# Kernel tuning notes

Measured on AMD Instinct MI355X. Metric: run time of the kernel, lower is better.

## Reference

```python
import jax, jax.numpy as jnp
import numpy as np

C = 192   # channels (class attr)
N = 196   # tokens per stream; 2N = 392, R feat dim = 784
B = 256

def _pw(x, w, b):
    # 1x1 Conv1d == pointwise channel mix: x [B,Ci,L] -> [B,Co,L]
    return jnp.einsum('oi,bil->bol', w, x) + b[None, :, None]

def _bn(x, g, beta, m, v):
    # eval-mode BatchNorm1d
    inv = g / jnp.sqrt(v + 1e-5)
    return (x - m[None, :, None]) * inv[None, :, None] + beta[None, :, None]

def setup_inputs():
    key = jax.random.key(0)
    ks = jax.random.split(key, 24)
    s = 1.0 / np.sqrt(C)
    d = {}
    d['x'] = jax.random.normal(ks[0], (B, N, C), dtype=jnp.float32)
    d['y'] = jax.random.normal(ks[1], (B, N, C), dtype=jnp.float32)
    # linear_conv_1: Conv1d(C,C,1) + BN + ReLU
    d['w1'] = jax.random.normal(ks[2], (C, C), dtype=jnp.float32) * s
    d['b1'] = jax.random.normal(ks[3], (C,), dtype=jnp.float32) * 0.01
    d['g1'] = jnp.ones((C,), jnp.float32)
    d['be1'] = jnp.zeros((C,), jnp.float32)
    d['m1'] = jax.random.normal(ks[4], (C,), dtype=jnp.float32) * 0.1
    d['v1'] = jax.random.uniform(ks[5], (C,), dtype=jnp.float32) + 0.5
    # linear_conv_2
    d['w2'] = jax.random.normal(ks[6], (C, C), dtype=jnp.float32) * s
    d['b2'] = jax.random.normal(ks[7], (C,), dtype=jnp.float32) * 0.01
    d['g2'] = jnp.ones((C,), jnp.float32)
    d['be2'] = jnp.zeros((C,), jnp.float32)
    d['m2'] = jax.random.normal(ks[8], (C,), dtype=jnp.float32) * 0.1
    d['v2'] = jax.random.uniform(ks[9], (C,), dtype=jnp.float32) + 0.5
    # linear_conv_3: Conv1d(C,C,1)
    d['w3'] = jax.random.normal(ks[10], (C, C), dtype=jnp.float32) * s
    d['b3'] = jax.random.normal(ks[11], (C,), dtype=jnp.float32) * 0.01
    # linear_conv_4: Conv1d(784,784,1)
    d['w4'] = jax.random.normal(ks[12], (784, 784), dtype=jnp.float32) / np.sqrt(784)
    d['b4'] = jax.random.normal(ks[13], (784,), dtype=jnp.float32) * 0.01
    # linear_conv_5: Conv1d(C+784,1,1)
    d['w5'] = jax.random.normal(ks[14], (1, C + 784), dtype=jnp.float32) / np.sqrt(C + 784)
    d['b5'] = jax.random.normal(ks[15], (1,), dtype=jnp.float32) * 0.01
    return d

def reference(x, y, w1, b1, g1, be1, m1, v1, w2, b2, g2, be2, m2, v2, w3, b3, w4, b4, w5, b5):
    xp = jnp.swapaxes(x, 1, 2)  # [B,C,N]
    yp = jnp.swapaxes(y, 1, 2)
    phi_x = jax.nn.relu(_bn(_pw(xp, w1, b1), g1, be1, m1, v1))
    phi_y = jax.nn.relu(_bn(_pw(yp, w2, b2), g2, be2, m2, v2))
    cat_phi = jnp.concatenate([phi_x, phi_y], axis=2)            # [B,C,2N]
    A = jnp.einsum('bcn,bcm->bnm', cat_phi, cat_phi)             # [B,2N,2N]
    # R[b,i,:] = cat(A[b,i,:], A[b,:,i]) for i in 0..2N-1, then permute(0,2,1)
    R = jnp.concatenate([A, jnp.swapaxes(A, 1, 2)], axis=2)      # [B,2N,4N]
    R = jnp.swapaxes(R, 1, 2)                                    # [B,4N,2N] = [B,784,392]
    v = _pw(cat_phi, w3, b3)                                     # [B,C,392]
    v_ = _pw(R, w4, b4)                                          # [B,784,392]
    cat_v = jnp.concatenate([v, v_], axis=1)                     # [B,976,392]
    W = _pw(cat_v, w5, b5)                                       # [B,1,392]
    out = xp * W[:, :, :N] + yp * W[:, :, N:]                    # [B,C,N]
    return out
```

## Files before the change

### kernel.cpp

```cpp
#include <hip/hip_runtime.h>
#include <hip/hip_bf16.h>

typedef __attribute__((ext_vector_type(8))) short bf16x8;
typedef __attribute__((ext_vector_type(4))) float f32x4;

#define CDIM 192
#define NTOK 196
#define LTOT 392
#define NBE 64

__device__ __forceinline__ ushort f2bf(float f) {
  uint u = __float_as_uint(f);
  u = (u + 0x7FFFu + ((u >> 16) & 1u)) >> 16;
  return (ushort)u;
}
__device__ __forceinline__ float bf2f(ushort h) {
  return __uint_as_float(((uint)h) << 16);
}
__device__ __forceinline__ uint pk2(float lo, float hi) {
  __hip_bfloat162 t = __float22bfloat162_rn(float2{lo, hi});
  uint r;
  __builtin_memcpy(&r, &t, 4);
  return r;
}
__device__ __forceinline__ float wave_reduce(float a) {
#pragma unroll
  for (int off = 32; off > 0; off >>= 1) a += __shfl_xor(a, off);
  return a;
}
__device__ __forceinline__ void barL() {
  asm volatile("s_waitcnt lgkmcnt(0)" ::: "memory");
  __builtin_amdgcn_s_barrier();
  __builtin_amdgcn_sched_barrier(0);
}

__global__ __launch_bounds__(256) void prep_kernel(
    const float* __restrict__ w1, const float* __restrict__ b1, const float* __restrict__ g1,
    const float* __restrict__ be1, const float* __restrict__ m1, const float* __restrict__ v1,
    const float* __restrict__ w2, const float* __restrict__ b2, const float* __restrict__ g2,
    const float* __restrict__ be2, const float* __restrict__ m2, const float* __restrict__ v2,
    const float* __restrict__ w3, const float* __restrict__ b3,
    const float* __restrict__ w4, const float* __restrict__ b4,
    const float* __restrict__ w5, const float* __restrict__ b5,
    ushort* __restrict__ w1b, ushort* __restrict__ w2b,
    float* __restrict__ u3, float* __restrict__ u4, float* __restrict__ cvecs,
    float* __restrict__ Kc) {
  const int bid = blockIdx.x;
  const int wid = threadIdx.x >> 6, lane = threadIdx.x & 63;
  if (bid < NBE) {
    for (int i = bid * 256 + threadIdx.x; i < 74112; i += NBE * 256) {
      if (i < 36864) {
        int o = i / CDIM;
        float inv = g1[o] * rsqrtf(v1[o] + 1e-5f);
        w1b[i] = f2bf(w1[i] * inv);
      } else if (i < 73728) {
        int j = i - 36864; int o = j / CDIM;
        float inv = g2[o] * rsqrtf(v2[o] + 1e-5f);
        w2b[j] = f2bf(w2[j] * inv);
      } else {
        int k = i - 73728; int h = k / CDIM, o = k % CDIM;
        const float* bb = h ? b2 : b1; const float* gg = h ? g2 : g1;
        const float* bee = h ? be2 : be1;
        const float* mm = h ? m2 : m1; const float* vv = h ? v2 : v1;
        float inv = gg[o] * rsqrtf(vv[o] + 1e-5f);
        cvecs[k] = (bb[o] - mm[o]) * inv + bee[o];
      }
    }
  } else if (bid < NBE + 48) {
    int j = (bid - NBE) * 4 + wid;
    float a = 0.f;
    for (int c = lane; c < CDIM; c += 64) a += w5[c] * w3[c * CDIM + j];
    a = wave_reduce(a);
    if (lane == 0) u3[j] = a;
  } else if (bid < NBE + 48 + 98) {
    int j = (bid - NBE - 48) * 4 + wid;
    float a = 0.f;
    for (int o = lane; o < 784; o += 64)
      a += w5[CDIM + o] * (w4[o * 784 + j] + w4[o * 784 + j + LTOT]);
    a = wave_reduce(a);
    if (lane == 0) u4[j] = a;
  } else {
    if (wid == 0) {
      float a = 0.f;
      for (int i = lane; i < CDIM + 784; i += 64)
        a += (i < CDIM) ? w5[i] * b3[i] : w5[i] * b4[i - CDIM];
      a = wave_reduce(a);
      if (lane == 0) Kc[0] = a + b5[0];
    }
  }
}

#define PHIL_BYTES (404 * 384)
#define OFF_U4S PHIL_BYTES
#define OFF_CSL (OFF_U4S + 1600)
#define OFF_SARR (OFF_CSL + 1536)
#define SMEM_BYTES (OFF_SARR + 768)

extern __shared__ char smem[];

__global__ __launch_bounds__(768, 1) void fused_kernel(
    const float* __restrict__ x, const float* __restrict__ y,
    const ushort* __restrict__ w1b, const ushort* __restrict__ w2b,
    const float* __restrict__ cvecs, const float* __restrict__ u4,
    const float* __restrict__ u3, const float* __restrict__ Kc,
    float* __restrict__ Wg) {
  const int b = blockIdx.x;
  ushort* phiL = (ushort*)smem;
  float* u4s = (float*)(smem + OFF_U4S);
  float* csL = (float*)(smem + OFF_CSL);
  float* sArr = (float*)(smem + OFF_SARR);
  const int tid = threadIdx.x;
  for (int i = tid; i < 400; i += 768) u4s[i] = (i < LTOT) ? u4[i] : 0.f;
  for (int i = tid; i < 384; i += 768) csL[i] = cvecs[i];

  const int w = tid >> 6, lane = tid & 63;
  const int lrow = lane & 15, kgrp = lane >> 4;
  const int c = w * 16 + lrow;

  bf16x8 bfr0[6], bfr1[6];
#pragma unroll
  for (int kk = 0; kk < 6; kk++) {
    bfr0[kk] = *(const bf16x8*)(w1b + (size_t)c * CDIM + kk * 32 + kgrp * 8);
    bfr1[kk] = *(const bf16x8*)(w2b + (size_t)c * CDIM + kk * 32 + kgrp * 8);
  }
  barL();
  const float csr0 = csL[c], csr1 = csL[CDIM + c];

  const float4* xb4 = (const float4*)(x + (size_t)b * NTOK * CDIM);
  const float4* yb4 = (const float4*)(y + (size_t)b * NTOK * CDIM);
  float sp = 0.f;

  auto loadpf = [&](int R, float4* pf) {
    if (R < 14) {
      const float4* s4 = (R < 7) ? xb4 : yb4;
      const int base = (R % 7) * 1536;
#pragma unroll
      for (int p = 0; p < 2; p++) {
        const int fi = base + p * 768 + tid;
        pf[p] = (fi < 9408) ? s4[fi] : float4{0.f, 0.f, 0.f, 0.f};
      }
    }
  };
  float4 pfA[2], pfB[2];
  loadpf(0, pfA);
  loadpf(1, pfB);

  for (int R = 0; R < 14; R++) {
    const int h = R / 7, r = R % 7;
#pragma unroll
    for (int p = 0; p < 2; p++) {
      const int fi = r * 1536 + p * 768 + tid;
      if (fi < 9408) {
        const int row = fi / 48, c4 = fi - row * 48;
        const int l = h * NTOK + row;
        uint2 wv;
        wv.x = pk2(pfA[p].x, pfA[p].y);
        wv.y = pk2(pfA[p].z, pfA[p].w);
        uint addr = (uint)(l * 384 + c4 * 8) ^ (uint)((l & 7) << 4);
        *(uint2*)((char*)phiL + addr) = wv;
      }
    }
    pfA[0] = pfB[0]; pfA[1] = pfB[1];
    loadpf(R + 2, pfB);
    barL();

    const bool t1ok = (r * 32 + 16) < NTOK;
    f32x4 acc0 = {0.f, 0.f, 0.f, 0.f}, acc1 = {0.f, 0.f, 0.f, 0.f};
    {
      bf16x8 a0[6], a1[6];
      const int l0 = h * NTOK + r * 32 + lrow;
#pragma unroll
      for (int kk = 0; kk < 6; kk++) {
        uint ad0 = (uint)(l0 * 384 + (kk * 32 + kgrp * 8) * 2) ^ (uint)((l0 & 7) << 4);
        a0[kk] = *(const bf16x8*)((const char*)phiL + ad0);
        const int l1 = l0 + 16;
        uint ad1 = (uint)(l1 * 384 + (kk * 32 + kgrp * 8) * 2) ^ (uint)((l1 & 7) << 4);
        a1[kk] = *(const bf16x8*)((const char*)phiL + ad1);
      }
      if (h == 0) {
#pragma unroll
        for (int kk = 0; kk < 6; kk++) {
          acc0 = __builtin_amdgcn_mfma_f32_16x16x32_bf16(a0[kk], bfr0[kk], acc0, 0, 0, 0);
          if (t1ok) acc1 = __builtin_amdgcn_mfma_f32_16x16x32_bf16(a1[kk], bfr0[kk], acc1, 0, 0, 0);
        }
      } else {
#pragma unroll
        for (int kk = 0; kk < 6; kk++) {
          acc0 = __builtin_amdgcn_mfma_f32_16x16x32_bf16(a0[kk], bfr1[kk], acc0, 0, 0, 0);
          if (t1ok) acc1 = __builtin_amdgcn_mfma_f32_16x16x32_bf16(a1[kk], bfr1[kk], acc1, 0, 0, 0);
        }
      }
    }
    barL();

    {
      const float csr = h ? csr1 : csr0;
#pragma unroll
      for (int tt = 0; tt < 2; tt++) {
        const int rb = r * 32 + tt * 16;
        if (rb < NTOK) {
          const f32x4 ac = tt ? acc1 : acc0;
          const float v0 = fmaxf(ac[0] + csr, 0.f);
          const float v1 = fmaxf(ac[1] + csr, 0.f);
          const float v2 = fmaxf(ac[2] + csr, 0.f);
          const float v3 = fmaxf(ac[3] + csr, 0.f);
          const uint p01 = pk2(v0, v1), p23 = pk2(v2, v3);
          const int row0 = rb + 4 * kgrp;
#pragma unroll
          for (int j = 0; j < 4; j++) {
            const int row = row0 + j;
            if (row < NTOK) {
              const int l = h * NTOK + row;
              uint addr = (uint)(l * 384 + c * 2) ^ (uint)((l & 7) << 4);
              const uint piece = (j == 0) ? (p01 & 0xFFFFu) : (j == 1) ? (p01 >> 16)
                               : (j == 2) ? (p23 & 0xFFFFu) : (p23 >> 16);
              *(ushort*)((char*)phiL + addr) = (ushort)piece;
              const float vj = (j == 0) ? v0 : (j == 1) ? v1 : (j == 2) ? v2 : v3;
              sp += u4s[l] * vj;
            }
          }
        }
      }
    }
  }

  sp += __shfl_xor(sp, 16);
  sp += __shfl_xor(sp, 32);
  if (kgrp == 0) sArr[c] = sp;
  barL();
  for (int i = tid; i < CDIM; i += 768) sArr[i] = u3[i] + sArr[i];
  barL();

  const float Kv = Kc[0];
  const int grp = tid >> 2, g4 = tid & 3;
  for (int l = grp; l < LTOT; l += 192) {
    float acc = 0.f;
#pragma unroll
    for (int q = 0; q < 12; q++) {
      const int cc = g4 * 48 + q * 4;
      uint addr = (uint)(l * 384 + cc * 2) ^ (uint)((l & 7) << 4);
      ushort4 v = *(const ushort4*)((const char*)phiL + addr);
      acc += sArr[cc] * bf2f(v.x) + sArr[cc + 1] * bf2f(v.y) +
             sArr[cc + 2] * bf2f(v.z) + sArr[cc + 3] * bf2f(v.w);
    }
    acc += __shfl_xor(acc, 1);
    acc += __shfl_xor(acc, 2);
    if (g4 == 0) Wg[b * LTOT + l] = acc + Kv;
  }
}

__global__ __launch_bounds__(256) void out_kernel(
    const float* __restrict__ x, const float* __restrict__ y,
    const float* __restrict__ Wg, float* __restrict__ out) {
  const int bid = blockIdx.x;
  const int b = bid / 7, nt = bid % 7;
  const int n0 = nt * 28;
  __shared__ float Wl[56];
  __shared__ float tile[28][193];
  const int tid = threadIdx.x;
  if (tid < 56) {
    const int lg = (tid < 28) ? (n0 + tid) : (NTOK + n0 + tid - 28);
    Wl[tid] = Wg[b * LTOT + lg];
  }
  __syncthreads();
  for (int i = tid; i < 28 * 48; i += 256) {
    const int nl = i / 48, c4 = (i % 48) * 4;
    const size_t xi = ((size_t)b * NTOK + n0 + nl) * CDIM + c4;
    const float4 xv = *(const float4*)&x[xi];
    const float4 yv = *(const float4*)&y[xi];
    const float wx = Wl[nl], wy = Wl[28 + nl];
    tile[nl][c4 + 0] = xv.x * wx + yv.x * wy;
    tile[nl][c4 + 1] = xv.y * wx + yv.y * wy;
    tile[nl][c4 + 2] = xv.z * wx + yv.z * wy;
    tile[nl][c4 + 3] = xv.w * wx + yv.w * wy;
  }
  __syncthreads();
  for (int i = tid; i < CDIM * 7; i += 256) {
    const int c = i / 7, nq = i % 7;
    float4 o;
    o.x = tile[nq * 4 + 0][c]; o.y = tile[nq * 4 + 1][c];
    o.z = tile[nq * 4 + 2][c]; o.w = tile[nq * 4 + 3][c];
    *(float4*)&out[((size_t)b * CDIM + c) * NTOK + n0 + nq * 4] = o;
  }
}

extern "C" void kernel_launch(void* const* d_in, const int* in_sizes, int n_in,
                              void* d_out, int out_size, void* d_ws, size_t ws_size,
                              hipStream_t stream) {
  const float* x   = (const float*)d_in[0];
  const float* y   = (const float*)d_in[1];
  const float* w1  = (const float*)d_in[2];
  const float* b1  = (const float*)d_in[3];
  const float* g1  = (const float*)d_in[4];
  const float* be1 = (const float*)d_in[5];
  const float* m1  = (const float*)d_in[6];
  const float* v1  = (const float*)d_in[7];
  const float* w2  = (const float*)d_in[8];
  const float* b2  = (const float*)d_in[9];
  const float* g2  = (const float*)d_in[10];
  const float* be2 = (const float*)d_in[11];
  const float* m2  = (const float*)d_in[12];
  const float* v2  = (const float*)d_in[13];
  const float* w3  = (const float*)d_in[14];
  const float* b3  = (const float*)d_in[15];
  const float* w4  = (const float*)d_in[16];
  const float* b4  = (const float*)d_in[17];
  const float* w5  = (const float*)d_in[18];
  const float* b5  = (const float*)d_in[19];
  float* out = (float*)d_out;

  char* ws = (char*)d_ws;
  ushort* w1b  = (ushort*)ws;
  ushort* w2b  = (ushort*)(ws + 73728);
  float* fbase = (float*)(ws + 147456);
  float* u3    = fbase;
  float* u4    = fbase + 192;
  float* cvecs = fbase + 584;
  float* Kc    = fbase + 968;
  float* Wg    = fbase + 976;

  prep_kernel<<<211, 256, 0, stream>>>(w1, b1, g1, be1, m1, v1,
                                       w2, b2, g2, be2, m2, v2,
                                       w3, b3, w4, b4, w5, b5,
                                       w1b, w2b, u3, u4, cvecs, Kc);
  fused_kernel<<<256, 768, SMEM_BYTES, stream>>>(x, y, w1b, w2b, cvecs, u4,
                                                 u3, Kc, Wg);
  out_kernel<<<256 * 7, 256, 0, stream>>>(x, y, Wg, out);
}
```

Baseline: 63.42 us.

## Fuse output scaling into main kernel and widen per-round row tiles

Removes the separate out_kernel launch: the fused kernel keeps the per-token gate W in shared memory and itself computes out = x*Wx + y*Wy, then transposes through a padded LDS tile with prefetched x/y loads. The phi projection loop also shifts from 14 rounds of 32 rows to 8 rounds of 64 rows, each round handling four 16-row MFMA tiles. This saves a kernel launch, the global round-trip of Wg and fewer barriers. In exchange the output phase now runs on only 256 blocks instead of 1792, which may lower memory-level parallelism, and register pressure rises.

```diff
diff --git a/kernel.cpp b/kernel.cpp
--- a/kernel.cpp
+++ b/kernel.cpp
@@ -92,9 +92,10 @@
 
 #define PHIL_BYTES (404 * 384)
 #define OFF_U4S PHIL_BYTES
-#define OFF_CSL (OFF_U4S + 1600)
+#define OFF_CSL (OFF_U4S + 1632)
 #define OFF_SARR (OFF_CSL + 1536)
-#define SMEM_BYTES (OFF_SARR + 768)
+#define OFF_WL (OFF_SARR + 768)
+#define SMEM_BYTES (OFF_WL + 1568)
 
 extern __shared__ char smem[];
 
@@ -103,14 +104,15 @@
     const ushort* __restrict__ w1b, const ushort* __restrict__ w2b,
     const float* __restrict__ cvecs, const float* __restrict__ u4,
     const float* __restrict__ u3, const float* __restrict__ Kc,
-    float* __restrict__ Wg) {
+    float* __restrict__ out) {
   const int b = blockIdx.x;
   ushort* phiL = (ushort*)smem;
   float* u4s = (float*)(smem + OFF_U4S);
   float* csL = (float*)(smem + OFF_CSL);
   float* sArr = (float*)(smem + OFF_SARR);
+  float* Wl = (float*)(smem + OFF_WL);
   const int tid = threadIdx.x;
-  for (int i = tid; i < 400; i += 768) u4s[i] = (i < LTOT) ? u4[i] : 0.f;
+  for (int i = tid; i < 408; i += 768) u4s[i] = (i < LTOT) ? u4[i] : 0.f;
   for (int i = tid; i < 384; i += 768) csL[i] = cvecs[i];
 
   const int w = tid >> 6, lane = tid & 63;
@@ -131,25 +133,25 @@
   float sp = 0.f;
 
   auto loadpf = [&](int R, float4* pf) {
-    if (R < 14) {
-      const float4* s4 = (R < 7) ? xb4 : yb4;
-      const int base = (R % 7) * 1536;
-#pragma unroll
-      for (int p = 0; p < 2; p++) {
+    if (R < 8) {
+      const float4* s4 = (R < 4) ? xb4 : yb4;
+      const int base = (R & 3) * 3072;
+#pragma unroll
+      for (int p = 0; p < 4; p++) {
         const int fi = base + p * 768 + tid;
         pf[p] = (fi < 9408) ? s4[fi] : float4{0.f, 0.f, 0.f, 0.f};
       }
     }
   };
-  float4 pfA[2], pfB[2];
+  float4 pfA[4], pfB[4];
   loadpf(0, pfA);
   loadpf(1, pfB);
 
-  for (int R = 0; R < 14; R++) {
-    const int h = R / 7, r = R % 7;
-#pragma unroll
-    for (int p = 0; p < 2; p++) {
-      const int fi = r * 1536 + p * 768 + tid;
+  for (int R = 0; R < 8; R++) {
+    const int h = R >> 2, r = R & 3;
+#pragma unroll
+    for (int p = 0; p < 4; p++) {
+      const int fi = r * 3072 + p * 768 + tid;
       if (fi < 9408) {
         const int row = fi / 48, c4 = fi - row * 48;
         const int l = h * NTOK + row;
@@ -160,64 +162,60 @@
         *(uint2*)((char*)phiL + addr) = wv;
       }
     }
-    pfA[0] = pfB[0]; pfA[1] = pfB[1];
+#pragma unroll
+    for (int p = 0; p < 4; p++) pfA[p] = pfB[p];
     loadpf(R + 2, pfB);
     barL();
 
-    const bool t1ok = (r * 32 + 16) < NTOK;
-    f32x4 acc0 = {0.f, 0.f, 0.f, 0.f}, acc1 = {0.f, 0.f, 0.f, 0.f};
-    {
-      bf16x8 a0[6], a1[6];
-      const int l0 = h * NTOK + r * 32 + lrow;
-#pragma unroll
-      for (int kk = 0; kk < 6; kk++) {
-        uint ad0 = (uint)(l0 * 384 + (kk * 32 + kgrp * 8) * 2) ^ (uint)((l0 & 7) << 4);
-        a0[kk] = *(const bf16x8*)((const char*)phiL + ad0);
-        const int l1 = l0 + 16;
-        uint ad1 = (uint)(l1 * 384 + (kk * 32 + kgrp * 8) * 2) ^ (uint)((l1 & 7) << 4);
-        a1[kk] = *(const bf16x8*)((const char*)phiL + ad1);
-      }
-      if (h == 0) {
+    f32x4 acc[4];
+#pragma unroll
+    for (int tt = 0; tt < 4; tt++) acc[tt] = f32x4{0.f, 0.f, 0.f, 0.f};
+#pragma unroll
+    for (int tt = 0; tt < 4; tt++) {
+      const int rb = r * 64 + tt * 16;
+      if (rb < NTOK) {
+        bf16x8 af[6];
+        const int l0 = h * NTOK + rb + lrow;
 #pragma unroll
         for (int kk = 0; kk < 6; kk++) {
-          acc0 = __builtin_amdgcn_mfma_f32_16x16x32_bf16(a0[kk], bfr0[kk], acc0, 0, 0, 0);
-          if (t1ok) acc1 = __builtin_amdgcn_mfma_f32_16x16x32_bf16(a1[kk], bfr0[kk], acc1, 0, 0, 0);
+          uint ad = (uint)(l0 * 384 + (kk * 32 + kgrp * 8) * 2) ^ (uint)((l0 & 7) << 4);
+          af[kk] = *(const bf16x8*)((const char*)phiL + ad);
         }
-      } else {
-#pragma unroll
-        for (int kk = 0; kk < 6; kk++) {
-          acc0 = __builtin_amdgcn_mfma_f32_16x16x32_bf16(a0[kk], bfr1[kk], acc0, 0, 0, 0);
-          if (t1ok) acc1 = __builtin_amdgcn_mfma_f32_16x16x32_bf16(a1[kk], bfr1[kk], acc1, 0, 0, 0);
+        if (h == 0) {
+#pragma unroll
+          for (int kk = 0; kk < 6; kk++)
+            acc[tt] = __builtin_amdgcn_mfma_f32_16x16x32_bf16(af[kk], bfr0[kk], acc[tt], 0, 0, 0);
+        } else {
+#pragma unroll
+          for (int kk = 0; kk < 6; kk++)
+            acc[tt] = __builtin_amdgcn_mfma_f32_16x16x32_bf16(af[kk], bfr1[kk], acc[tt], 0, 0, 0);
         }
       }
     }
     barL();
 
-    {
-      const float csr = h ? csr1 : csr0;
-#pragma unroll
-      for (int tt = 0; tt < 2; tt++) {
-        const int rb = r * 32 + tt * 16;
-        if (rb < NTOK) {
-          const f32x4 ac = tt ? acc1 : acc0;
-          const float v0 = fmaxf(ac[0] + csr, 0.f);
-          const float v1 = fmaxf(ac[1] + csr, 0.f);
-          const float v2 = fmaxf(ac[2] + csr, 0.f);
-          const float v3 = fmaxf(ac[3] + csr, 0.f);
-          const uint p01 = pk2(v0, v1), p23 = pk2(v2, v3);
-          const int row0 = rb + 4 * kgrp;
-#pragma unroll
-          for (int j = 0; j < 4; j++) {
-            const int row = row0 + j;
-            if (row < NTOK) {
-              const int l = h * NTOK + row;
-              uint addr = (uint)(l * 384 + c * 2) ^ (uint)((l & 7) << 4);
-              const uint piece = (j == 0) ? (p01 & 0xFFFFu) : (j == 1) ? (p01 >> 16)
-                               : (j == 2) ? (p23 & 0xFFFFu) : (p23 >> 16);
-              *(ushort*)((char*)phiL + addr) = (ushort)piece;
-              const float vj = (j == 0) ? v0 : (j == 1) ? v1 : (j == 2) ? v2 : v3;
-              sp += u4s[l] * vj;
-            }
+    const float csr = h ? csr1 : csr0;
+#pragma unroll
+    for (int tt = 0; tt < 4; tt++) {
+      const int rb = r * 64 + tt * 16;
+      if (rb < NTOK) {
+        const float v0 = fmaxf(acc[tt][0] + csr, 0.f);
+        const float v1 = fmaxf(acc[tt][1] + csr, 0.f);
+        const float v2 = fmaxf(acc[tt][2] + csr, 0.f);
+        const float v3 = fmaxf(acc[tt][3] + csr, 0.f);
+        const uint p01 = pk2(v0, v1), p23 = pk2(v2, v3);
+        const int row0 = rb + 4 * kgrp;
+#pragma unroll
+        for (int j = 0; j < 4; j++) {
+          const int row = row0 + j;
+          if (row < NTOK) {
+            const int l = h * NTOK + row;
+            uint addr = (uint)(l * 384 + c * 2) ^ (uint)((l & 7) << 4);
+            const uint piece = (j == 0) ? (p01 & 0xFFFFu) : (j == 1) ? (p01 >> 16)
+                             : (j == 2) ? (p23 & 0xFFFFu) : (p23 >> 16);
+            *(ushort*)((char*)phiL + addr) = (ushort)piece;
+            const float vj = (j == 0) ? v0 : (j == 1) ? v1 : (j == 2) ? v2 : v3;
+            sp += u4s[l] * vj;
           }
         }
       }
@@ -245,42 +243,57 @@
     }
     acc += __shfl_xor(acc, 1);
     acc += __shfl_xor(acc, 2);
-    if (g4 == 0) Wg[b * LTOT + l] = acc + Kv;
-  }
-}
-
-__global__ __launch_bounds__(256) void out_kernel(
-    const float* __restrict__ x, const float* __restrict__ y,
-    const float* __restrict__ Wg, float* __restrict__ out) {
-  const int bid = blockIdx.x;
-  const int b = bid / 7, nt = bid % 7;
-  const int n0 = nt * 28;
-  __shared__ float Wl[56];
-  __shared__ float tile[28][193];
-  const int tid = threadIdx.x;
-  if (tid < 56) {
-    const int lg = (tid < 28) ? (n0 + tid) : (NTOK + n0 + tid - 28);
-    Wl[tid] = Wg[b * LTOT + lg];
-  }
-  __syncthreads();
-  for (int i = tid; i < 28 * 48; i += 256) {
-    const int nl = i / 48, c4 = (i % 48) * 4;
-    const size_t xi = ((size_t)b * NTOK + n0 + nl) * CDIM + c4;
-    const float4 xv = *(const float4*)&x[xi];
-    const float4 yv = *(const float4*)&y[xi];
-    const float wx = Wl[nl], wy = Wl[28 + nl];
-    tile[nl][c4 + 0] = xv.x * wx + yv.x * wy;
-    tile[nl][c4 + 1] = xv.y * wx + yv.y * wy;
-    tile[nl][c4 + 2] = xv.z * wx + yv.z * wy;
-    tile[nl][c4 + 3] = xv.w * wx + yv.w * wy;
-  }
-  __syncthreads();
-  for (int i = tid; i < CDIM * 7; i += 256) {
-    const int c = i / 7, nq = i % 7;
-    float4 o;
-    o.x = tile[nq * 4 + 0][c]; o.y = tile[nq * 4 + 1][c];
-    o.z = tile[nq * 4 + 2][c]; o.w = tile[nq * 4 + 3][c];
-    *(float4*)&out[((size_t)b * CDIM + c) * NTOK + n0 + nq * 4] = o;
+    if (g4 == 0) Wl[l] = acc + Kv;
+  }
+
+  float* tileF = (float*)smem;
+  const float* xb = x + (size_t)b * NTOK * CDIM;
+  const float* yb = y + (size_t)b * NTOK * CDIM;
+  float4 px[2], py[2];
+  auto loadT = [&](int nt) {
+    if (nt < 7) {
+#pragma unroll
+      for (int p = 0; p < 2; p++) {
+        const int i = p * 768 + tid;
+        if (i < 1344) {
+          const size_t xi = (size_t)(nt * 28 + i / 48) * CDIM + (i % 48) * 4;
+          px[p] = *(const float4*)&xb[xi];
+          py[p] = *(const float4*)&yb[xi];
+        }
+      }
+    }
+  };
+  loadT(0);
+  for (int nt = 0; nt < 7; nt++) {
+    const int n0 = nt * 28;
+    barL();
+#pragma unroll
+    for (int p = 0; p < 2; p++) {
+      const int i = p * 768 + tid;
+      if (i < 1344) {
+        const int nl = i / 48, c4 = (i % 48) * 4;
+        const float wx = Wl[n0 + nl], wy = Wl[NTOK + n0 + nl];
+        tileF[nl * 193 + c4 + 0] = px[p].x * wx + py[p].x * wy;
+        tileF[nl * 193 + c4 + 1] = px[p].y * wx + py[p].y * wy;
+        tileF[nl * 193 + c4 + 2] = px[p].z * wx + py[p].z * wy;
+        tileF[nl * 193 + c4 + 3] = px[p].w * wx + py[p].w * wy;
+      }
+    }
+    loadT(nt + 1);
+    barL();
+#pragma unroll
+    for (int p = 0; p < 2; p++) {
+      const int i = p * 768 + tid;
+      if (i < 1344) {
+        const int cc = i / 7, nq = i % 7;
+        float4 o;
+        o.x = tileF[(nq * 4 + 0) * 193 + cc];
+        o.y = tileF[(nq * 4 + 1) * 193 + cc];
+        o.z = tileF[(nq * 4 + 2) * 193 + cc];
+        o.w = tileF[(nq * 4 + 3) * 193 + cc];
+        *(float4*)&out[((size_t)b * CDIM + cc) * NTOK + n0 + nq * 4] = o;
+      }
+    }
   }
 }
 
@@ -317,13 +330,11 @@
   float* u4    = fbase + 192;
   float* cvecs = fbase + 584;
   float* Kc    = fbase + 968;
-  float* Wg    = fbase + 976;
 
   prep_kernel<<<211, 256, 0, stream>>>(w1, b1, g1, be1, m1, v1,
                                        w2, b2, g2, be2, m2, v2,
                                        w3, b3, w4, b4, w5, b5,
                                        w1b, w2b, u3, u4, cvecs, Kc);
   fused_kernel<<<256, 768, SMEM_BYTES, stream>>>(x, y, w1b, w2b, cvecs, u4,
-                                                 u3, Kc, Wg);
-  out_kernel<<<256 * 7, 256, 0, stream>>>(x, y, Wg, out);
-}
+                                                 u3, Kc, out);
+}
```

New measurement: 61.37 us. -3.2%, faster.

## Split fused per-batch kernel into two 1024-block phi passes with recompute

Applied to the files above, without the earlier changes.

Replaces the single 256-block fused kernel, which kept all of phi in shared memory, with two kernels, each launched as 1024 blocks split by batch, stream and token half. The first computes the u4-weighted partial sums of phi. The second recomputes phi with 32x32x16 MFMAs and reduces it against the combined channel coefficients to produce Wg. The aim is to fill the GPU with more, smaller blocks and drop the large shared-memory footprint. The cost is reading x and y twice, doing the phi GEMM twice, and one extra launch.

```diff
diff --git a/kernel.cpp b/kernel.cpp
--- a/kernel.cpp
+++ b/kernel.cpp
@@ -2,7 +2,7 @@
 #include <hip/hip_bf16.h>
 
 typedef __attribute__((ext_vector_type(8))) short bf16x8;
-typedef __attribute__((ext_vector_type(4))) float f32x4;
+typedef __attribute__((ext_vector_type(16))) float f32x16;
 
 #define CDIM 192
 #define NTOK 196
@@ -90,162 +90,173 @@
   }
 }
 
-#define PHIL_BYTES (404 * 384)
-#define OFF_U4S PHIL_BYTES
-#define OFF_CSL (OFF_U4S + 1600)
-#define OFF_SARR (OFF_CSL + 1536)
-#define SMEM_BYTES (OFF_SARR + 768)
-
-extern __shared__ char smem[];
-
-__global__ __launch_bounds__(768, 1) void fused_kernel(
+__device__ __constant__ int L0S[2][4] = {{0, 32, 64, -1}, {96, 128, 160, 164}};
+
+__global__ __launch_bounds__(384) void phis_kernel(
     const float* __restrict__ x, const float* __restrict__ y,
     const ushort* __restrict__ w1b, const ushort* __restrict__ w2b,
     const float* __restrict__ cvecs, const float* __restrict__ u4,
-    const float* __restrict__ u3, const float* __restrict__ Kc,
+    float* __restrict__ s_part) {
+  const int bid = blockIdx.x;
+  const int b = bid >> 2, h = (bid >> 1) & 1, g = bid & 1;
+  const float4* src4 = (const float4*)(((h ? y : x) + (size_t)b * NTOK * CDIM));
+  const ushort* wb = h ? w2b : w1b;
+  __shared__ ushort Abuf[2][32 * CDIM];
+  __shared__ float u4s[100];
+  const int tid = threadIdx.x;
+  const int rbase = g ? 96 : 0;
+  for (int i = tid; i < 100; i += 384) u4s[i] = u4[h * NTOK + rbase + i];
+
+  const int w = tid >> 6, lane = tid & 63;
+  const int cl32 = lane & 31, hi = lane >> 5;
+  const int c = w * 32 + cl32;
+
+  bf16x8 bfr[12];
+#pragma unroll
+  for (int kk = 0; kk < 12; kk++)
+    bfr[kk] = *(const bf16x8*)(wb + (size_t)c * CDIM + kk * 16 + hi * 8);
+  const float csr = cvecs[h * CDIM + c];
+
+  const int nchunks = g ? 4 : 3;
+  float sp = 0.f;
+  float4 pf[4];
+#pragma unroll
+  for (int p = 0; p < 4; p++) pf[p] = src4[L0S[g][0] * 48 + p * 384 + tid];
+
+  for (int k = 0; k < 4; k++) {
+    if (k >= nchunks) break;
+    const int l0 = L0S[g][k];
+    ushort* Ab = &Abuf[k & 1][0];
+#pragma unroll
+    for (int p = 0; p < 4; p++) {
+      const int fi = p * 384 + tid;
+      const int r = fi / 48, c4 = fi % 48;
+      uint2 wv;
+      wv.x = pk2(pf[p].x, pf[p].y);
+      wv.y = pk2(pf[p].z, pf[p].w);
+      uint addr = (uint)(r * 384 + c4 * 8) ^ (uint)((r & 7) << 4);
+      *(uint2*)((char*)Ab + addr) = wv;
+    }
+    if (k + 1 < nchunks) {
+#pragma unroll
+      for (int p = 0; p < 4; p++)
+        pf[p] = src4[L0S[g][k + 1] * 48 + p * 384 + tid];
+    }
+    __builtin_amdgcn_sched_barrier(0);
+    barL();
+    f32x16 acc;
+#pragma unroll
+    for (int e = 0; e < 16; e++) acc[e] = 0.f;
+    const uint swz = (uint)((cl32 & 7) << 4);
+    __builtin_amdgcn_s_setprio(1);
+#pragma unroll
+    for (int kk = 0; kk < 12; kk++) {
+      uint ad = (uint)(cl32 * 384 + kk * 32 + hi * 16) ^ swz;
+      bf16x8 af = *(const bf16x8*)((const char*)Ab + ad);
+      acc = __builtin_amdgcn_mfma_f32_32x32x16_bf16(af, bfr[kk], acc, 0, 0, 0);
+    }
+    __builtin_amdgcn_s_setprio(0);
+    const bool ovl = (l0 == 164);
+#pragma unroll
+    for (int e = 0; e < 16; e++) {
+      const int rl = (e & 3) + 8 * (e >> 2) + 4 * hi;
+      const int row = l0 + rl;
+      if (!ovl || row >= 192) {
+        const float v = fmaxf(acc[e] + csr, 0.f);
+        sp += u4s[row - rbase] * v;
+      }
+    }
+  }
+  sp += __shfl_xor(sp, 32);
+  if (hi == 0) s_part[(size_t)((b * 2 + h) * 2 + g) * CDIM + c] = sp;
+}
+
+__global__ __launch_bounds__(384) void wrec_kernel(
+    const float* __restrict__ x, const float* __restrict__ y,
+    const ushort* __restrict__ w1b, const ushort* __restrict__ w2b,
+    const float* __restrict__ cvecs, const float* __restrict__ u3,
+    const float* __restrict__ s_part, const float* __restrict__ Kc,
     float* __restrict__ Wg) {
-  const int b = blockIdx.x;
-  ushort* phiL = (ushort*)smem;
-  float* u4s = (float*)(smem + OFF_U4S);
-  float* csL = (float*)(smem + OFF_CSL);
-  float* sArr = (float*)(smem + OFF_SARR);
+  const int bid = blockIdx.x;
+  const int b = bid >> 2, h = (bid >> 1) & 1, g = bid & 1;
+  const float4* src4 = (const float4*)(((h ? y : x) + (size_t)b * NTOK * CDIM));
+  const ushort* wb = h ? w2b : w1b;
+  __shared__ ushort Abuf[2][32 * CDIM];
+  __shared__ float Wred[6][32];
   const int tid = threadIdx.x;
-  for (int i = tid; i < 400; i += 768) u4s[i] = (i < LTOT) ? u4[i] : 0.f;
-  for (int i = tid; i < 384; i += 768) csL[i] = cvecs[i];
-
   const int w = tid >> 6, lane = tid & 63;
-  const int lrow = lane & 15, kgrp = lane >> 4;
-  const int c = w * 16 + lrow;
-
-  bf16x8 bfr0[6], bfr1[6];
-#pragma unroll
-  for (int kk = 0; kk < 6; kk++) {
-    bfr0[kk] = *(const bf16x8*)(w1b + (size_t)c * CDIM + kk * 32 + kgrp * 8);
-    bfr1[kk] = *(const bf16x8*)(w2b + (size_t)c * CDIM + kk * 32 + kgrp * 8);
-  }
-  barL();
-  const float csr0 = csL[c], csr1 = csL[CDIM + c];
-
-  const float4* xb4 = (const float4*)(x + (size_t)b * NTOK * CDIM);
-  const float4* yb4 = (const float4*)(y + (size_t)b * NTOK * CDIM);
-  float sp = 0.f;
-
-  auto loadpf = [&](int R, float4* pf) {
-    if (R < 14) {
-      const float4* s4 = (R < 7) ? xb4 : yb4;
-      const int base = (R % 7) * 1536;
-#pragma unroll
-      for (int p = 0; p < 2; p++) {
-        const int fi = base + p * 768 + tid;
-        pf[p] = (fi < 9408) ? s4[fi] : float4{0.f, 0.f, 0.f, 0.f};
+  const int cl32 = lane & 31, hi = lane >> 5;
+  const int c = w * 32 + cl32;
+
+  bf16x8 bfr[12];
+#pragma unroll
+  for (int kk = 0; kk < 12; kk++)
+    bfr[kk] = *(const bf16x8*)(wb + (size_t)c * CDIM + kk * 16 + hi * 8);
+  const float csr = cvecs[h * CDIM + c];
+  float cf = u3[c];
+#pragma unroll
+  for (int q = 0; q < 4; q++) cf += s_part[(size_t)(b * 4 + q) * CDIM + c];
+  const float Kv = Kc[0];
+
+  const int nchunks = g ? 4 : 3;
+  float4 pf[4];
+#pragma unroll
+  for (int p = 0; p < 4; p++) pf[p] = src4[L0S[g][0] * 48 + p * 384 + tid];
+
+  for (int k = 0; k < 4; k++) {
+    if (k >= nchunks) break;
+    const int l0 = L0S[g][k];
+    ushort* Ab = &Abuf[k & 1][0];
+#pragma unroll
+    for (int p = 0; p < 4; p++) {
+      const int fi = p * 384 + tid;
+      const int r = fi / 48, c4 = fi % 48;
+      uint2 wv;
+      wv.x = pk2(pf[p].x, pf[p].y);
+      wv.y = pk2(pf[p].z, pf[p].w);
+      uint addr = (uint)(r * 384 + c4 * 8) ^ (uint)((r & 7) << 4);
+      *(uint2*)((char*)Ab + addr) = wv;
+    }
+    if (k + 1 < nchunks) {
+#pragma unroll
+      for (int p = 0; p < 4; p++)
+        pf[p] = src4[L0S[g][k + 1] * 48 + p * 384 + tid];
+    }
+    __builtin_amdgcn_sched_barrier(0);
+    barL();
+    f32x16 acc;
+#pragma unroll
+    for (int e = 0; e < 16; e++) acc[e] = 0.f;
+    const uint swz = (uint)((cl32 & 7) << 4);
+    __builtin_amdgcn_s_setprio(1);
+#pragma unroll
+    for (int kk = 0; kk < 12; kk++) {
+      uint ad = (uint)(cl32 * 384 + kk * 32 + hi * 16) ^ swz;
+      bf16x8 af = *(const bf16x8*)((const char*)Ab + ad);
+      acc = __builtin_amdgcn_mfma_f32_32x32x16_bf16(af, bfr[kk], acc, 0, 0, 0);
+    }
+    __builtin_amdgcn_s_setprio(0);
+    float pv[16];
+#pragma unroll
+    for (int e = 0; e < 16; e++) pv[e] = fmaxf(acc[e] + csr, 0.f) * cf;
+#pragma unroll
+    for (int m = 1; m <= 16; m <<= 1)
+#pragma unroll
+      for (int e = 0; e < 16; e++) pv[e] += __shfl_xor(pv[e], m);
+    if (cl32 == 0) {
+#pragma unroll
+      for (int e = 0; e < 16; e++) {
+        const int rl = (e & 3) + 8 * (e >> 2) + 4 * hi;
+        Wred[w][rl] = pv[e];
       }
     }
-  };
-  float4 pfA[2], pfB[2];
-  loadpf(0, pfA);
-  loadpf(1, pfB);
-
-  for (int R = 0; R < 14; R++) {
-    const int h = R / 7, r = R % 7;
-#pragma unroll
-    for (int p = 0; p < 2; p++) {
-      const int fi = r * 1536 + p * 768 + tid;
-      if (fi < 9408) {
-        const int row = fi / 48, c4 = fi - row * 48;
-        const int l = h * NTOK + row;
-        uint2 wv;
-        wv.x = pk2(pfA[p].x, pfA[p].y);
-        wv.y = pk2(pfA[p].z, pfA[p].w);
-        uint addr = (uint)(l * 384 + c4 * 8) ^ (uint)((l & 7) << 4);
-        *(uint2*)((char*)phiL + addr) = wv;
-      }
-    }
-    pfA[0] = pfB[0]; pfA[1] = pfB[1];
-    loadpf(R + 2, pfB);
     barL();
-
-    const bool t1ok = (r * 32 + 16) < NTOK;
-    f32x4 acc0 = {0.f, 0.f, 0.f, 0.f}, acc1 = {0.f, 0.f, 0.f, 0.f};
-    {
-      bf16x8 a0[6], a1[6];
-      const int l0 = h * NTOK + r * 32 + lrow;
-#pragma unroll
-      for (int kk = 0; kk < 6; kk++) {
-        uint ad0 = (uint)(l0 * 384 + (kk * 32 + kgrp * 8) * 2) ^ (uint)((l0 & 7) << 4);
-        a0[kk] = *(const bf16x8*)((const char*)phiL + ad0);
-        const int l1 = l0 + 16;
-        uint ad1 = (uint)(l1 * 384 + (kk * 32 + kgrp * 8) * 2) ^ (uint)((l1 & 7) << 4);
-        a1[kk] = *(const bf16x8*)((const char*)phiL + ad1);
-      }
-      if (h == 0) {
-#pragma unroll
-        for (int kk = 0; kk < 6; kk++) {
-          acc0 = __builtin_amdgcn_mfma_f32_16x16x32_bf16(a0[kk], bfr0[kk], acc0, 0, 0, 0);
-          if (t1ok) acc1 = __builtin_amdgcn_mfma_f32_16x16x32_bf16(a1[kk], bfr0[kk], acc1, 0, 0, 0);
-        }
-      } else {
-#pragma unroll
-        for (int kk = 0; kk < 6; kk++) {
-          acc0 = __builtin_amdgcn_mfma_f32_16x16x32_bf16(a0[kk], bfr1[kk], acc0, 0, 0, 0);
-          if (t1ok) acc1 = __builtin_amdgcn_mfma_f32_16x16x32_bf16(a1[kk], bfr1[kk], acc1, 0, 0, 0);
-        }
-      }
-    }
-    barL();
-
-    {
-      const float csr = h ? csr1 : csr0;
-#pragma unroll
-      for (int tt = 0; tt < 2; tt++) {
-        const int rb = r * 32 + tt * 16;
-        if (rb < NTOK) {
-          const f32x4 ac = tt ? acc1 : acc0;
-          const float v0 = fmaxf(ac[0] + csr, 0.f);
-          const float v1 = fmaxf(ac[1] + csr, 0.f);
-          const float v2 = fmaxf(ac[2] + csr, 0.f);
-          const float v3 = fmaxf(ac[3] + csr, 0.f);
-          const uint p01 = pk2(v0, v1), p23 = pk2(v2, v3);
-          const int row0 = rb + 4 * kgrp;
-#pragma unroll
-          for (int j = 0; j < 4; j++) {
-            const int row = row0 + j;
-            if (row < NTOK) {
-              const int l = h * NTOK + row;
-              uint addr = (uint)(l * 384 + c * 2) ^ (uint)((l & 7) << 4);
-              const uint piece = (j == 0) ? (p01 & 0xFFFFu) : (j == 1) ? (p01 >> 16)
-                               : (j == 2) ? (p23 & 0xFFFFu) : (p23 >> 16);
-              *(ushort*)((char*)phiL + addr) = (ushort)piece;
-              const float vj = (j == 0) ? v0 : (j == 1) ? v1 : (j == 2) ? v2 : v3;
-              sp += u4s[l] * vj;
-            }
-          }
-        }
-      }
-    }
-  }
-
-  sp += __shfl_xor(sp, 16);
-  sp += __shfl_xor(sp, 32);
-  if (kgrp == 0) sArr[c] = sp;
-  barL();
-  for (int i = tid; i < CDIM; i += 768) sArr[i] = u3[i] + sArr[i];
-  barL();
-
-  const float Kv = Kc[0];
-  const int grp = tid >> 2, g4 = tid & 3;
-  for (int l = grp; l < LTOT; l += 192) {
-    float acc = 0.f;
-#pragma unroll
-    for (int q = 0; q < 12; q++) {
-      const int cc = g4 * 48 + q * 4;
-      uint addr = (uint)(l * 384 + cc * 2) ^ (uint)((l & 7) << 4);
-      ushort4 v = *(const ushort4*)((const char*)phiL + addr);
-      acc += sArr[cc] * bf2f(v.x) + sArr[cc + 1] * bf2f(v.y) +
-             sArr[cc + 2] * bf2f(v.z) + sArr[cc + 3] * bf2f(v.w);
-    }
-    acc += __shfl_xor(acc, 1);
-    acc += __shfl_xor(acc, 2);
-    if (g4 == 0) Wg[b * LTOT + l] = acc + Kv;
+    if (tid < 32) {
+      float sw = 0.f;
+#pragma unroll
+      for (int ww = 0; ww < 6; ww++) sw += Wred[ww][tid];
+      Wg[b * LTOT + h * NTOK + l0 + tid] = sw + Kv;
+    }
   }
 }
 
@@ -317,13 +328,14 @@
   float* u4    = fbase + 192;
   float* cvecs = fbase + 584;
   float* Kc    = fbase + 968;
-  float* Wg    = fbase + 976;
+  float* s_part = fbase + 976;
+  float* Wg    = fbase + 976 + 196608;
 
   prep_kernel<<<211, 256, 0, stream>>>(w1, b1, g1, be1, m1, v1,
                                        w2, b2, g2, be2, m2, v2,
                                        w3, b3, w4, b4, w5, b5,
                                        w1b, w2b, u3, u4, cvecs, Kc);
-  fused_kernel<<<256, 768, SMEM_BYTES, stream>>>(x, y, w1b, w2b, cvecs, u4,
-                                                 u3, Kc, Wg);
+  phis_kernel<<<1024, 384, 0, stream>>>(x, y, w1b, w2b, cvecs, u4, s_part);
+  wrec_kernel<<<1024, 384, 0, stream>>>(x, y, w1b, w2b, cvecs, u3, s_part, Kc, Wg);
   out_kernel<<<256 * 7, 256, 0, stream>>>(x, y, Wg, out);
 }
```

Result: slower. 107.1 us (+68.8%).
